# Kernel tuning notes

Measured on AMD Instinct MI355X. Metric: run time of the kernel, lower is better.

The kernel has to match this reference:

```python
import jax, jax.numpy as jnp
import numpy as np

S, I, H, O = 8192, 1024, 1024, 1024


def setup_inputs() -> dict:
    key = jax.random.key(0)
    ks = jax.random.split(key, 7)
    s = 1.0 / np.sqrt(H).astype(np.float32)  # PyTorch LSTM/Linear init scale
    u = lambda k, shape: jax.random.uniform(k, shape, jnp.float32, -s, s)
    return {
        "x": jax.random.normal(ks[0], (S, I), jnp.float32),
        "W_ih": u(ks[1], (4 * H, I)),   # gate order: i, f, g, o (PyTorch)
        "W_hh": u(ks[2], (4 * H, H)),
        "b_ih": u(ks[3], (4 * H,)),
        "b_hh": u(ks[4], (4 * H,)),
        "W_out": u(ks[5], (O, H)),
        "b_out": u(ks[6], (O,)),
    }


def _lstm_forward(x, W_ih, W_hh, b_ih, b_hh, W_out, b_out):
    h_dim = W_hh.shape[1]
    # Precompute input projections for all timesteps in one GEMM: [S, 4H]
    x_proj = x @ W_ih.T + (b_ih + b_hh)

    def step(carry, xp_t):
        h, c = carry                       # [H], [H]
        gates = xp_t + h @ W_hh.T          # [4H]
        i, f, g, o = jnp.split(gates, 4)
        i = jax.nn.sigmoid(i)
        f = jax.nn.sigmoid(f)
        g = jnp.tanh(g)
        o = jax.nn.sigmoid(o)
        c = f * c + i * g
        h = o * jnp.tanh(c)
        return (h, c), h

    init = (jnp.zeros((h_dim,), x.dtype), jnp.zeros((h_dim,), x.dtype))
    _, hs = jax.lax.scan(step, init, x_proj)   # hs: [S, H]
    logits = hs @ W_out.T + b_out              # [S, O]
    return jax.nn.log_softmax(logits, axis=1)


def reference(x, W_ih, W_hh, b_ih, b_hh, W_out, b_out):
    return _lstm_forward(x, W_ih, W_hh, b_ih, b_hh, W_out, b_out)
```

## Files before the change

kernel.cpp:

```cpp
#include <hip/hip_runtime.h>


using u16 = unsigned short;
using u32 = unsigned int;
using u64 = unsigned long long;

typedef short  short8  __attribute__((ext_vector_type(8)));
typedef float  floatx4 __attribute__((ext_vector_type(4)));
typedef u32    uintx4  __attribute__((ext_vector_type(4)));

#define S_LEN 8192
#define NPROD 64

__device__ __forceinline__ u16 f2bf(float f) {
    u32 u = __float_as_uint(f);
    u += 0x7FFFu + ((u >> 16) & 1u);
    return (u16)(u >> 16);
}

__device__ __forceinline__ floatx4 mfma16(short8 a, short8 b, floatx4 c) {
    return __builtin_amdgcn_mfma_f32_16x16x32_bf16(a, b, c, 0, 0, 0);
}


__global__ void cvt_f32_bf16(const float* __restrict__ src, u16* __restrict__ dst, int n) {
    for (int i = blockIdx.x * blockDim.x + threadIdx.x; i < n; i += gridDim.x * blockDim.x)
        dst[i] = f2bf(src[i]);
}

__global__ void bias_comb_k(const float* __restrict__ a, const float* __restrict__ b,
                            float* __restrict__ o) {
    int i = blockIdx.x * blockDim.x + threadIdx.x;
    if (i < 4096) o[i] = a[i] + b[i];
}

__global__ void init_hbuf(u64* __restrict__ hbuf) {
    hbuf[blockIdx.x * 256 + threadIdx.x] = 0ull;
}


__global__ __launch_bounds__(256) void gemm_bt(const u16* __restrict__ A,
                                               const u16* __restrict__ B,
                                               const float* __restrict__ bias,
                                               float* __restrict__ C,
                                               int M, int N, int K) {
    const int tid = threadIdx.x;
    const int l = tid & 63, w = tid >> 6;
    const int m0 = blockIdx.x * 128 + (w >> 1) * 64;
    const int n0 = blockIdx.y * 64 + (w & 1) * 32;
    const int lr = l & 15, lk = (l >> 4) * 8;

    floatx4 acc[4][2];
#pragma unroll
    for (int i = 0; i < 4; i++)
#pragma unroll
        for (int j = 0; j < 2; j++) acc[i][j] = floatx4{0.f, 0.f, 0.f, 0.f};

    const u16* Ap = A + (size_t)(m0 + lr) * K + lk;
    const u16* Bp = B + (size_t)(n0 + lr) * K + lk;

    for (int k0 = 0; k0 < K; k0 += 32) {
        short8 a0 = *(const short8*)(Ap + k0);
        short8 a1 = *(const short8*)(Ap + (size_t)16 * K + k0);
        short8 a2 = *(const short8*)(Ap + (size_t)32 * K + k0);
        short8 a3 = *(const short8*)(Ap + (size_t)48 * K + k0);
        short8 b0 = *(const short8*)(Bp + k0);
        short8 b1 = *(const short8*)(Bp + (size_t)16 * K + k0);
        acc[0][0] = mfma16(a0, b0, acc[0][0]); acc[0][1] = mfma16(a0, b1, acc[0][1]);
        acc[1][0] = mfma16(a1, b0, acc[1][0]); acc[1][1] = mfma16(a1, b1, acc[1][1]);
        acc[2][0] = mfma16(a2, b0, acc[2][0]); acc[2][1] = mfma16(a2, b1, acc[2][1]);
        acc[3][0] = mfma16(a3, b0, acc[3][0]); acc[3][1] = mfma16(a3, b1, acc[3][1]);
    }

    const int rr = (l >> 4) * 4;
#pragma unroll
    for (int j = 0; j < 2; j++) {
        const int n = n0 + j * 16 + lr;
        const float bv = bias[n];
#pragma unroll
        for (int i = 0; i < 4; i++) {
            const int m = m0 + i * 16 + rr;
#pragma unroll
            for (int r = 0; r < 4; r++)
                C[(size_t)(m + r) * N + n] = acc[i][j][r] + bv;
        }
    }
}


__device__ __forceinline__ float sig_f(float x) {
    return __builtin_amdgcn_rcpf(1.f + __expf(-x));
}
__device__ __forceinline__ float tanh_f(float x) {
    return 1.f - 2.f * __builtin_amdgcn_rcpf(1.f + __expf(2.f * x));
}

__global__ __launch_bounds__(512, 2) void lstm_rec(const u16* __restrict__ Whhb,
                                                   const float* __restrict__ xp,
                                                   u64* __restrict__ hbuf,
                                                   u32* __restrict__ hs) {
    const int p = blockIdx.x;
    const int tid = threadIdx.x;
    const int l = tid & 63, w = tid >> 6;
    const int g = w & 3;
    const int kh = w >> 2;

    __shared__ u32 h_lds[512];
    __shared__ float dots[128];

    short8 afr[16];
    {
        const u16* wr = Whhb + (size_t)(g * 1024 + p * 16 + (l & 15)) * 1024
                       + kh * 512 + ((l >> 4) * 8);
#pragma unroll
        for (int kb = 0; kb < 16; ++kb) afr[kb] = *(const short8*)(wr + kb * 32);
    }
    h_lds[tid] = 0u;

    float c_state = 0.f;
    const float* xprow = xp + (size_t)(l >> 4) * 1024 + p * 16 + (l & 15);
    float xpn = (w == 0) ? xprow[0] : 0.f;
    __syncthreads();

    const int bofs = (l >> 4) * 4;
    const u32* hb_base = &h_lds[kh * 256 + bofs];

    for (int t = 0; t < S_LEN; ++t) {
        float xc = xpn;
        if (w == 0) {
            int tn = (t + 1 < S_LEN) ? t + 1 : S_LEN - 1;
            xpn = xprow[(size_t)tn * 4096];
        }

        if (t > 0) {
            u64* src = hbuf + (size_t)(t & 1) * 512 + tid;
            u64 v;
            do {
                v = __hip_atomic_load(src, __ATOMIC_RELAXED, __HIP_MEMORY_SCOPE_AGENT);
            } while ((u32)(v >> 32) != (u32)t);
            h_lds[tid] = (u32)v;
        }
        __syncthreads();

        floatx4 ac0 = floatx4{0,0,0,0}, ac1 = floatx4{0,0,0,0};
        floatx4 ac2 = floatx4{0,0,0,0}, ac3 = floatx4{0,0,0,0};
#pragma unroll
        for (int kb = 0; kb < 16; kb += 4) {
            uintx4 b0 = *(const uintx4*)(hb_base + (kb + 0) * 16);
            uintx4 b1 = *(const uintx4*)(hb_base + (kb + 1) * 16);
            uintx4 b2 = *(const uintx4*)(hb_base + (kb + 2) * 16);
            uintx4 b3 = *(const uintx4*)(hb_base + (kb + 3) * 16);
            ac0 = mfma16(afr[kb + 0], __builtin_bit_cast(short8, b0), ac0);
            ac1 = mfma16(afr[kb + 1], __builtin_bit_cast(short8, b1), ac1);
            ac2 = mfma16(afr[kb + 2], __builtin_bit_cast(short8, b2), ac2);
            ac3 = mfma16(afr[kb + 3], __builtin_bit_cast(short8, b3), ac3);
        }
        floatx4 acs = (ac0 + ac1) + (ac2 + ac3);
        if ((l & 15) == 0) {
            const int q = l >> 4;
#pragma unroll
            for (int r = 0; r < 4; ++r) dots[kh * 64 + g * 16 + q * 4 + r] = acs[r];
        }
        __syncthreads();

        if (w == 0) {
            float a = dots[l] + dots[64 + l] + xc;
            float act = ((l >> 4) == 2) ? tanh_f(a) : sig_f(a);
            const int jj = l & 15;
            float fi = __shfl(act, jj);
            float ff = __shfl(act, 16 + jj);
            float fg = __shfl(act, 32 + jj);
            float fo = __shfl(act, 48 + jj);
            if (l < 16) {
                c_state = ff * c_state + fi * fg;
                float h = fo * tanh_f(c_state);
                u16 hb16 = f2bf(h);
                u32 other = (u32)__shfl_down((int)hb16, 1);
                if ((l & 1) == 0) {
                    u32 pk = (u32)hb16 | (other << 16);
                    int pidx = p * 8 + (l >> 1);
                    u64 tv = ((u64)(u32)(t + 1) << 32) | (u64)pk;
                    __hip_atomic_store(&hbuf[(size_t)((t + 1) & 1) * 512 + pidx], tv,
                                       __ATOMIC_RELAXED, __HIP_MEMORY_SCOPE_AGENT);
                    hs[(size_t)t * 512 + pidx] = pk;
                }
            }
        }
    }
}


__global__ __launch_bounds__(256) void lsm_k(float* __restrict__ C) {
    const int tid = threadIdx.x;
    float* p = C + (size_t)blockIdx.x * 1024;
    float v0 = p[tid], v1 = p[tid + 256], v2 = p[tid + 512], v3 = p[tid + 768];
    float mx = fmaxf(fmaxf(v0, v1), fmaxf(v2, v3));
#pragma unroll
    for (int o = 1; o < 64; o <<= 1) mx = fmaxf(mx, __shfl_xor(mx, o));
    __shared__ float red[4];
    const int w = tid >> 6, l = tid & 63;
    if (l == 0) red[w] = mx;
    __syncthreads();
    mx = fmaxf(fmaxf(red[0], red[1]), fmaxf(red[2], red[3]));
    float s = __expf(v0 - mx) + __expf(v1 - mx) + __expf(v2 - mx) + __expf(v3 - mx);
#pragma unroll
    for (int o = 1; o < 64; o <<= 1) s += __shfl_xor(s, o);
    __syncthreads();
    if (l == 0) red[w] = s;
    __syncthreads();
    s = red[0] + red[1] + red[2] + red[3];
    float ls = __logf(s) + mx;
    p[tid] = v0 - ls; p[tid + 256] = v1 - ls; p[tid + 512] = v2 - ls; p[tid + 768] = v3 - ls;
}


extern "C" void kernel_launch(void* const* d_in, const int* in_sizes, int n_in,
                              void* d_out, int out_size, void* d_ws, size_t ws_size,
                              hipStream_t stream) {
    const float* x     = (const float*)d_in[0];
    const float* W_ih  = (const float*)d_in[1];
    const float* W_hh  = (const float*)d_in[2];
    const float* b_ih  = (const float*)d_in[3];
    const float* b_hh  = (const float*)d_in[4];
    const float* W_out = (const float*)d_in[5];
    const float* b_out = (const float*)d_in[6];

    char* ws = (char*)d_ws;
    u16*   xb    = (u16*)(ws + 0);
    u16*   Wihb  = (u16*)(ws + 16777216);
    u16*   Whhb  = (u16*)(ws + 25165824);
    u16*   Woutb = (u16*)(ws + 33554432);
    float* biasc = (float*)(ws + 35651584);
    u64*   hbuf  = (u64*)(ws + 35667968);
    u32*   hs    = (u32*)(ws + 35676160);
    float* xp    = (float*)(ws + 52453376);

    init_hbuf<<<4, 256, 0, stream>>>(hbuf);
    cvt_f32_bf16<<<2048, 256, 0, stream>>>(x, xb, 8192 * 1024);
    cvt_f32_bf16<<<1024, 256, 0, stream>>>(W_ih, Wihb, 4096 * 1024);
    cvt_f32_bf16<<<1024, 256, 0, stream>>>(W_hh, Whhb, 4096 * 1024);
    cvt_f32_bf16<<<256, 256, 0, stream>>>(W_out, Woutb, 1024 * 1024);
    bias_comb_k<<<16, 256, 0, stream>>>(b_ih, b_hh, biasc);

    gemm_bt<<<dim3(64, 64), 256, 0, stream>>>(xb, Wihb, biasc, xp, 8192, 4096, 1024);

    lstm_rec<<<NPROD, 512, 0, stream>>>(Whhb, xp, hbuf, hs);

    gemm_bt<<<dim3(64, 16), 256, 0, stream>>>((const u16*)hs, Woutb, b_out, (float*)d_out,
                                              8192, 1024, 1024);

    lsm_k<<<8192, 256, 0, stream>>>((float*)d_out);
}
```

Measured before the change: 13.19 ms.

## Co-locate recurrent producers on one XCD and use non-coherent polling

Launches 512 blocks of the recurrent kernel and has each block read its XCC_ID, then claim a slot atomically. The first XCD to collect 64 blocks wins and runs the recurrence, so all producers share one L2 and exchange h through it with sc0 loads and plain stores instead of device-scope atomics. A timeout fallback assigns producers across XCDs if no XCD fills up. It also moves the xp prefetch and the hs writeback to wave 1 so they stay off the critical wave 0 path. The cost is extra blocks that launch and exit immediately, and reliance on undocumented cache-scope behaviour for correctness.

```diff
diff --git a/kernel.cpp b/kernel.cpp
--- a/kernel.cpp
+++ b/kernel.cpp
@@ -10,7 +10,8 @@
 typedef u32    uintx4  __attribute__((ext_vector_type(4)));
 
 #define S_LEN 8192
-#define NPROD 64
+#define NOWIN 0xFFFFFFFFu
+#define FBACK 0x100u
 
 __device__ __forceinline__ u16 f2bf(float f) {
     u32 u = __float_as_uint(f);
@@ -34,8 +35,10 @@
     if (i < 4096) o[i] = a[i] + b[i];
 }
 
-__global__ void init_hbuf(u64* __restrict__ hbuf) {
+__global__ void init_hbuf(u64* __restrict__ hbuf, u32* __restrict__ claim) {
     hbuf[blockIdx.x * 256 + threadIdx.x] = 0ull;
+    if (blockIdx.x == 0 && threadIdx.x < 64)
+        claim[threadIdx.x] = (threadIdx.x == 32) ? NOWIN : 0u;
 }
 
 
@@ -95,11 +98,41 @@
     return 1.f - 2.f * __builtin_amdgcn_rcpf(1.f + __expf(2.f * x));
 }
 
-__global__ __launch_bounds__(512, 2) void lstm_rec(const u16* __restrict__ Whhb,
+__global__ __launch_bounds__(512, 4) void lstm_rec(const u16* __restrict__ Whhb,
                                                    const float* __restrict__ xp,
                                                    u64* __restrict__ hbuf,
-                                                   u32* __restrict__ hs) {
-    const int p = blockIdx.x;
+                                                   u32* __restrict__ hs,
+                                                   u32* __restrict__ claim) {
+    __shared__ int s_p;
+    __shared__ int s_fast;
+    if (threadIdx.x == 0) {
+        u32 xcd;
+        asm volatile("s_getreg_b32 %0, hwreg(HW_REG_XCC_ID)" : "=s"(xcd));
+        xcd &= 15u;
+        u32 slot = atomicAdd(&claim[xcd], 1u);
+        if (slot == 63u) atomicCAS(&claim[32], NOWIN, xcd);
+        u64 t0 = __builtin_amdgcn_s_memrealtime();
+        u32 win, spins = 0;
+        while ((win = __hip_atomic_load(&claim[32], __ATOMIC_RELAXED,
+                                        __HIP_MEMORY_SCOPE_AGENT)) == NOWIN) {
+            if (++spins > (1u << 20) ||
+                __builtin_amdgcn_s_memrealtime() - t0 > (1ull << 18))
+                atomicCAS(&claim[32], NOWIN, FBACK);
+        }
+        int p = -1, fast = 0;
+        if (win < 16u) {
+            if (xcd == win && slot < 64u) { p = (int)slot; fast = 1; }
+        } else {
+            u32 fs = atomicAdd(&claim[48], 1u);
+            if (fs < 64u) p = (int)fs;
+        }
+        s_p = p; s_fast = fast;
+    }
+    __syncthreads();
+    const int p = s_p;
+    const int fast = s_fast;
+    if (p < 0) return;
+
     const int tid = threadIdx.x;
     const int l = tid & 63, w = tid >> 6;
     const int g = w & 3;
@@ -107,6 +140,8 @@
 
     __shared__ u32 h_lds[512];
     __shared__ float dots[128];
+    __shared__ float xp_lds[2][64];
+    __shared__ u32 pk_lds[8];
 
     short8 afr[16];
     {
@@ -118,29 +153,76 @@
     h_lds[tid] = 0u;
 
     float c_state = 0.f;
-    const float* xprow = xp + (size_t)(l >> 4) * 1024 + p * 16 + (l & 15);
-    float xpn = (w == 0) ? xprow[0] : 0.f;
+    const float* xprow1 = xp + (size_t)(l >> 4) * 1024 + p * 16 + (l & 15);
+    float xv = 0.f;
+    if (w == 1) {
+        xp_lds[0][l] = xprow1[0];
+        xv = xprow1[4096];
+    }
     __syncthreads();
 
     const int bofs = (l >> 4) * 4;
     const u32* hb_base = &h_lds[kh * 256 + bofs];
 
     for (int t = 0; t < S_LEN; ++t) {
-        float xc = xpn;
-        if (w == 0) {
-            int tn = (t + 1 < S_LEN) ? t + 1 : S_LEN - 1;
-            xpn = xprow[(size_t)tn * 4096];
-        }
-
-        if (t > 0) {
-            u64* src = hbuf + (size_t)(t & 1) * 512 + tid;
-            u64 v;
-            do {
-                v = __hip_atomic_load(src, __ATOMIC_RELAXED, __HIP_MEMORY_SCOPE_AGENT);
-            } while ((u32)(v >> 32) != (u32)t);
-            h_lds[tid] = (u32)v;
+        if (t > 0 && w >= 1) {
+            const size_t par = (size_t)(t & 1) * 512;
+            u64* s1 = hbuf + par + (tid - 64);
+            u64 v1;
+            if (w == 7) {
+                u64* s2 = hbuf + par + 448 + l;
+                u64 v2;
+                if (fast) {
+                    u32 k = 0;
+                    do {
+                        if ((k++ & 3u) != 3u) {
+                            asm volatile("global_load_dwordx2 %0, %2, off sc0\n\t"
+                                         "global_load_dwordx2 %1, %3, off sc0\n\t"
+                                         "s_waitcnt vmcnt(0)"
+                                         : "=&v"(v1), "=&v"(v2)
+                                         : "v"(s1), "v"(s2) : "memory");
+                        } else {
+                            v1 = __hip_atomic_load(s1, __ATOMIC_RELAXED, __HIP_MEMORY_SCOPE_AGENT);
+                            v2 = __hip_atomic_load(s2, __ATOMIC_RELAXED, __HIP_MEMORY_SCOPE_AGENT);
+                        }
+                    } while ((u32)(v1 >> 32) != (u32)t || (u32)(v2 >> 32) != (u32)t);
+                } else {
+                    do {
+                        v1 = __hip_atomic_load(s1, __ATOMIC_RELAXED, __HIP_MEMORY_SCOPE_AGENT);
+                        v2 = __hip_atomic_load(s2, __ATOMIC_RELAXED, __HIP_MEMORY_SCOPE_AGENT);
+                    } while ((u32)(v1 >> 32) != (u32)t || (u32)(v2 >> 32) != (u32)t);
+                }
+                h_lds[tid - 64] = (u32)v1;
+                h_lds[448 + l]  = (u32)v2;
+            } else {
+                if (fast) {
+                    u32 k = 0;
+                    do {
+                        if ((k++ & 3u) != 3u) {
+                            asm volatile("global_load_dwordx2 %0, %1, off sc0\n\t"
+                                         "s_waitcnt vmcnt(0)"
+                                         : "=&v"(v1) : "v"(s1) : "memory");
+                        } else {
+                            v1 = __hip_atomic_load(s1, __ATOMIC_RELAXED, __HIP_MEMORY_SCOPE_AGENT);
+                        }
+                    } while ((u32)(v1 >> 32) != (u32)t);
+                } else {
+                    do {
+                        v1 = __hip_atomic_load(s1, __ATOMIC_RELAXED, __HIP_MEMORY_SCOPE_AGENT);
+                    } while ((u32)(v1 >> 32) != (u32)t);
+                }
+                h_lds[tid - 64] = (u32)v1;
+            }
         }
         __syncthreads();
+
+        if (w == 1) {
+            if (t > 0 && l < 8)
+                hs[(size_t)(t - 1) * 512 + p * 8 + l] = pk_lds[l];
+            xp_lds[(t + 1) & 1][l] = xv;
+            int tn = (t + 2 < S_LEN) ? t + 2 : S_LEN - 1;
+            xv = xprow1[(size_t)tn * 4096];
+        }
 
         floatx4 ac0 = floatx4{0,0,0,0}, ac1 = floatx4{0,0,0,0};
         floatx4 ac2 = floatx4{0,0,0,0}, ac3 = floatx4{0,0,0,0};
@@ -164,6 +246,7 @@
         __syncthreads();
 
         if (w == 0) {
+            float xc = xp_lds[t & 1][l];
             float a = dots[l] + dots[64 + l] + xc;
             float act = ((l >> 4) == 2) ? tanh_f(a) : sig_f(a);
             const int jj = l & 15;
@@ -179,14 +262,23 @@
                 if ((l & 1) == 0) {
                     u32 pk = (u32)hb16 | (other << 16);
                     int pidx = p * 8 + (l >> 1);
+                    pk_lds[l >> 1] = pk;
                     u64 tv = ((u64)(u32)(t + 1) << 32) | (u64)pk;
-                    __hip_atomic_store(&hbuf[(size_t)((t + 1) & 1) * 512 + pidx], tv,
-                                       __ATOMIC_RELAXED, __HIP_MEMORY_SCOPE_AGENT);
-                    hs[(size_t)t * 512 + pidx] = pk;
+                    u64* dst = &hbuf[(size_t)((t + 1) & 1) * 512 + pidx];
+                    asm volatile("s_waitcnt vmcnt(0)" ::: "memory");
+                    if (fast)
+                        asm volatile("global_store_dwordx2 %0, %1, off"
+                                     :: "v"(dst), "v"(tv) : "memory");
+                    __hip_atomic_store(dst, tv, __ATOMIC_RELAXED,
+                                       __HIP_MEMORY_SCOPE_AGENT);
                 }
             }
         }
     }
+
+    __syncthreads();
+    if (w == 1 && l < 8)
+        hs[(size_t)(S_LEN - 1) * 512 + p * 8 + l] = pk_lds[l];
 }
 
 
@@ -234,8 +326,9 @@
     u64*   hbuf  = (u64*)(ws + 35667968);
     u32*   hs    = (u32*)(ws + 35676160);
     float* xp    = (float*)(ws + 52453376);
-
-    init_hbuf<<<4, 256, 0, stream>>>(hbuf);
+    u32*   clm   = (u32*)(ws + 186671104);
+
+    init_hbuf<<<4, 256, 0, stream>>>(hbuf, clm);
     cvt_f32_bf16<<<2048, 256, 0, stream>>>(x, xb, 8192 * 1024);
     cvt_f32_bf16<<<1024, 256, 0, stream>>>(W_ih, Wihb, 4096 * 1024);
     cvt_f32_bf16<<<1024, 256, 0, stream>>>(W_hh, Whhb, 4096 * 1024);
@@ -244,7 +337,7 @@
 
     gemm_bt<<<dim3(64, 64), 256, 0, stream>>>(xb, Wihb, biasc, xp, 8192, 4096, 1024);
 
-    lstm_rec<<<NPROD, 512, 0, stream>>>(Whhb, xp, hbuf, hs);
+    lstm_rec<<<512, 512, 0, stream>>>(Whhb, xp, hbuf, hs, clm);
 
     gemm_bt<<<dim3(64, 16), 256, 0, stream>>>((const u16*)hs, Woutb, b_out, (float*)d_out,
                                               8192, 1024, 1024);
```

Result: slower. 19.89 ms (+50.7%).

## Poll h exchange with dwordx4 loads from four waves and stage xp in LDS

Applied to the files above, without the earlier changes.

The per-step poll of the global h buffer moves from all eight waves, each doing 64-bit atomic loads, to four waves issuing 128-bit system-coherent loads that cover two entries each, with an atomic-load fallback loop. The next-step x projection prefetch moves from wave 0 into a double-buffered LDS array filled by wave 5, so the gate wave reads it from LDS. The aim is fewer polling memory transactions on the recurrence critical path, and to take the global xp load latency off wave 0. The cost is reliance on inline asm and on the 128-bit load observing both tagged halves consistently.

```diff
diff --git a/kernel.cpp b/kernel.cpp
--- a/kernel.cpp
+++ b/kernel.cpp
@@ -107,6 +107,7 @@
 
     __shared__ u32 h_lds[512];
     __shared__ float dots[128];
+    __shared__ float xp_lds[2][64];
 
     short8 afr[16];
     {
@@ -119,26 +120,43 @@
 
     float c_state = 0.f;
     const float* xprow = xp + (size_t)(l >> 4) * 1024 + p * 16 + (l & 15);
-    float xpn = (w == 0) ? xprow[0] : 0.f;
+    if (w == 5) xp_lds[0][l] = xprow[0];
     __syncthreads();
 
     const int bofs = (l >> 4) * 4;
     const u32* hb_base = &h_lds[kh * 256 + bofs];
+    const int pi = (w - 1) * 64 + l;
 
     for (int t = 0; t < S_LEN; ++t) {
-        float xc = xpn;
+        float xc = 0.f;
+
         if (w == 0) {
+            xc = xp_lds[t & 1][l];
+        } else if (w == 5) {
             int tn = (t + 1 < S_LEN) ? t + 1 : S_LEN - 1;
-            xpn = xprow[(size_t)tn * 4096];
-        }
-
-        if (t > 0) {
-            u64* src = hbuf + (size_t)(t & 1) * 512 + tid;
-            u64 v;
-            do {
-                v = __hip_atomic_load(src, __ATOMIC_RELAXED, __HIP_MEMORY_SCOPE_AGENT);
-            } while ((u32)(v >> 32) != (u32)t);
-            h_lds[tid] = (u32)v;
+            xp_lds[(t + 1) & 1][l] = xprow[(size_t)tn * 4096];
+        } else if (w <= 4 && t > 0) {
+            u64* src0 = hbuf + (size_t)(t & 1) * 512 + 2 * pi;
+            const u32 want = (u32)t;
+            uintx4 q;
+            bool got = false;
+            for (int it = 0; it < 4096 && !got; ++it) {
+                asm volatile("global_load_dwordx4 %0, %1, off sc0 sc1\n\t"
+                             "s_waitcnt vmcnt(0)"
+                             : "=&v"(q) : "v"(src0) : "memory");
+                got = (q.y == want) && (q.w == want);
+            }
+            while (!got) {
+                u64 a = __hip_atomic_load(src0, __ATOMIC_RELAXED,
+                                          __HIP_MEMORY_SCOPE_AGENT);
+                u64 b = __hip_atomic_load(src0 + 1, __ATOMIC_RELAXED,
+                                          __HIP_MEMORY_SCOPE_AGENT);
+                if ((u32)(a >> 32) == want && (u32)(b >> 32) == want) {
+                    q.x = (u32)a; q.z = (u32)b; got = true;
+                }
+            }
+            h_lds[2 * pi]     = q.x;
+            h_lds[2 * pi + 1] = q.z;
         }
         __syncthreads();
 
```

Result: no change. 13.23 ms (+0.3%).
